# Kernel tuning notes

Measured on AMD Instinct MI355X. Metric: run time of the kernel, lower is better.

Reference implementation:

```python
import jax, jax.numpy as jnp
import numpy as np

N, E, B = 250000, 1000000, 500
FD = 78  # num_features_xd


def setup_inputs() -> dict:
    key = jax.random.key(0)
    ks = jax.random.split(key, 24)
    g = lambda i, shape, fan_in: jax.random.normal(ks[i], shape, jnp.float32) / np.sqrt(fan_in)
    inp = {
        "x": jax.random.normal(ks[0], (N, FD), jnp.float32),
        "edge_index": jax.random.randint(ks[1], (2, E), 0, N, jnp.int32),
        "batch": jnp.repeat(jnp.arange(B, dtype=jnp.int32), N // B),  # sorted, every graph non-empty
        "target": jax.random.randint(ks[2], (B, 1000), 0, 26, jnp.int32),
        # GCN layers
        "W1": g(3, (FD, FD), FD), "b1": jnp.zeros((FD,), jnp.float32),
        "W2": g(4, (FD, 2 * FD), FD), "b2": jnp.zeros((2 * FD,), jnp.float32),
        "W3": g(5, (2 * FD, 4 * FD), 2 * FD), "b3": jnp.zeros((4 * FD,), jnp.float32),
        # graph head
        "fcg1_w": g(6, (4 * FD, 1024), 4 * FD), "fcg1_b": jnp.zeros((1024,), jnp.float32),
        "fcg2_w": g(7, (1024, 128), 1024), "fcg2_b": jnp.zeros((128,), jnp.float32),
        # protein branch
        "emb": g(8, (26, 128), 1),
        "conv_w": g(9, (32, 1000, 8), 1000 * 8), "conv_b": jnp.zeros((32,), jnp.float32),
        "fcxt_w": g(10, (32 * 121, 128), 32 * 121), "fcxt_b": jnp.zeros((128,), jnp.float32),
        # fusion head
        "fc1_w": g(11, (256, 1024), 256), "fc1_b": jnp.zeros((1024,), jnp.float32),
        "fc2_w": g(12, (1024, 512), 1024), "fc2_b": jnp.zeros((512,), jnp.float32),
        "out_w": g(13, (512, 1), 512), "out_b": jnp.zeros((1,), jnp.float32),
    }
    return inp


def _gcn_conv(x, W, b, src, dst, dinv, n):
    # PyG GCNConv: out = D^-1/2 (A+I) D^-1/2 (x W) + b, symmetric norm with self-loops
    xw = x @ W
    norm = dinv[src] * dinv[dst]                                   # [E]
    agg = jax.ops.segment_sum(xw[src] * norm[:, None], dst, num_segments=n)
    agg = agg + xw * (dinv * dinv)[:, None]                        # self-loop term
    return agg + b


def reference(x, edge_index, batch, target,
              W1, b1, W2, b2, W3, b3,
              fcg1_w, fcg1_b, fcg2_w, fcg2_b,
              emb, conv_w, conv_b, fcxt_w, fcxt_b,
              fc1_w, fc1_b, fc2_w, fc2_b, out_w, out_b):
    n = x.shape[0]
    src, dst = edge_index[0], edge_index[1]
    # degree with self-loops (edge weights 1)
    deg = jax.ops.segment_sum(jnp.ones((src.shape[0],), x.dtype), dst, num_segments=n) + 1.0
    dinv = jax.lax.rsqrt(deg)

    h = jax.nn.relu(_gcn_conv(x, W1, b1, src, dst, dinv, n))
    h = jax.nn.relu(_gcn_conv(h, W2, b2, src, dst, dinv, n))
    h = jax.nn.relu(_gcn_conv(h, W3, b3, src, dst, dinv, n))

    bsz = fcg2_w.shape[1] * 0 + target.shape[0]  # B
    g = jax.ops.segment_max(h, batch, num_segments=bsz)            # global max pool -> [B, 312]
    g = jax.nn.relu(g @ fcg1_w + fcg1_b)
    g = g @ fcg2_w + fcg2_b                                        # dropout = identity (eval)

    # protein branch: Conv1d over embedding dim (channels = seq positions = 1000)
    e = emb[target]                                                # [B, 1000, 128]
    c = jax.lax.conv_general_dilated(e, conv_w, window_strides=(1,), padding="VALID",
                                     dimension_numbers=("NCH", "OIH", "NCH"))
    c = c + conv_b[None, :, None]                                  # [B, 32, 121]
    xt = c.reshape(bsz, 32 * 121) @ fcxt_w + fcxt_b

    xc = jnp.concatenate([g, xt], axis=1)                          # [B, 256]
    xc = jax.nn.relu(xc @ fc1_w + fc1_b)
    xc = jax.nn.relu(xc @ fc2_w + fc2_b)
    return xc @ out_w + out_b                                      # [B, 1]
```

## Files before the change

### kernel.cpp

```cpp
#include <hip/hip_runtime.h>
#include <hip/hip_bf16.h>

#define DEV_INLINE __device__ __forceinline__

static constexpr int Nn = 250000;
static constexpr int Ee = 1000000;
static constexpr int Bb = 500;
static constexpr int NPB = Nn / Bb;

typedef __attribute__((ext_vector_type(8))) short short8;
typedef __attribute__((ext_vector_type(8))) unsigned short ushort8v;
typedef __attribute__((ext_vector_type(4))) unsigned int uint4v;
typedef __attribute__((ext_vector_type(4))) float f32x4;
typedef __attribute__((ext_vector_type(2))) float f32x2;

DEV_INLINE __hip_bfloat16 f2b(float v) { return __float2bfloat16(v); }
DEV_INLINE unsigned short f2bu(float v) {
    __hip_bfloat16 h = __float2bfloat16(v);
    return __builtin_bit_cast(unsigned short, h);
}

DEV_INLINE f32x2 pairf(unsigned u) {
    f32x2 r;
    r.x = __uint_as_float(u << 16);
    r.y = __uint_as_float(u & 0xffff0000u);
    return r;
}
DEV_INLINE f32x2 fma2(f32x2 a, f32x2 b, f32x2 c) {
#if __has_builtin(__builtin_elementwise_fma)
    return __builtin_elementwise_fma(a, b, c);
#else
    return a * b + c;
#endif
}

__global__ void k_deg(const int* __restrict__ dst, int* __restrict__ deg) {
    int i = blockIdx.x * 256 + threadIdx.x;
    if (i < Ee) atomicAdd(&deg[dst[i]], 1);
}

__global__ void k_dinv(const int* __restrict__ deg, float* __restrict__ dinv) {
    int i = blockIdx.x * 256 + threadIdx.x;
    if (i < Nn) dinv[i] = rsqrtf((float)deg[i] + 1.0f);
}

__global__ __launch_bounds__(256) void k_scan1(const int* __restrict__ deg,
                                               int* __restrict__ rp,
                                               int* __restrict__ bsum) {
    __shared__ int s[256];
    int t = threadIdx.x;
    int i = blockIdx.x * 256 + t;
    int v = (i < Nn) ? deg[i] : 0;
    s[t] = v;
    __syncthreads();
    for (int off = 1; off < 256; off <<= 1) {
        int x = (t >= off) ? s[t - off] : 0;
        __syncthreads();
        s[t] += x;
        __syncthreads();
    }
    if (i < Nn) rp[i] = s[t] - v;
    if (t == 255) bsum[blockIdx.x] = s[255];
}

__global__ __launch_bounds__(1024) void k_scan2(int* __restrict__ bsum, int nb) {
    __shared__ int s[1024];
    int t = threadIdx.x;
    int v = (t < nb) ? bsum[t] : 0;
    s[t] = v;
    __syncthreads();
    for (int off = 1; off < 1024; off <<= 1) {
        int x = (t >= off) ? s[t - off] : 0;
        __syncthreads();
        s[t] += x;
        __syncthreads();
    }
    if (t < nb) bsum[t] = s[t] - v;
}

__global__ void k_scan3(int* __restrict__ rp, int* __restrict__ cursor,
                        const int* __restrict__ bsum) {
    int i = blockIdx.x * 256 + threadIdx.x;
    if (i < Nn) {
        int v = rp[i] + bsum[blockIdx.x];
        rp[i] = v;
        cursor[i] = v;
    }
    if (i == 0) rp[Nn] = Ee;
}

__global__ void k_scatter(const int* __restrict__ src, const int* __restrict__ dst,
                          const float* __restrict__ dinv, int* __restrict__ cursor,
                          int* __restrict__ col, float* __restrict__ enorm) {
    int i = blockIdx.x * 256 + threadIdx.x;
    if (i >= Ee) return;
    int s = src[i], d = dst[i];
    int pos = atomicAdd(&cursor[d], 1);
    col[pos] = s;
    enorm[pos] = dinv[s] * dinv[d];
}

__global__ void k_xprep(const float* __restrict__ x, unsigned short* __restrict__ xb) {
    int gid = blockIdx.x * 256 + threadIdx.x;
    if (gid >= Nn * 20) return;
    int i = gid / 20;
    int c = gid - 20 * i;
    int k = 4 * c;
    const float* xp = x + (size_t)i * 78;
    ushort4 u;
    u.x = (k + 0 < 78) ? f2bu(xp[k + 0]) : (unsigned short)0;
    u.y = (k + 1 < 78) ? f2bu(xp[k + 1]) : (unsigned short)0;
    u.z = (k + 2 < 78) ? f2bu(xp[k + 2]) : (unsigned short)0;
    u.w = (k + 3 < 78) ? f2bu(xp[k + 3]) : (unsigned short)0;
    *(ushort4*)&xb[(size_t)i * 80 + k] = u;
}

template <int K, int F, int KP, int FP>
__global__ __launch_bounds__(64) void k_wprep(const float* __restrict__ W,
                                              unsigned short* __restrict__ Wb) {
    constexpr int KSTEPS = KP / 32;
    const int nt = blockIdx.x, ks = blockIdx.y;
    const int l = threadIdx.x;
    const int n = nt * 16 + (l & 15);
    unsigned short* o = Wb + ((size_t)(nt * KSTEPS + ks) * 64 + l) * 8;
#pragma unroll
    for (int j = 0; j < 8; ++j) {
        const int k = (l >> 4) * 8 + j + ks * 32;
        o[j] = (k < K && n < F) ? f2bu(W[(size_t)k * F + n]) : (unsigned short)0;
    }
}

template <int KIN, int KP, int F, int FP, int SOUT, bool POOL, int MAXROWS>
__global__ __launch_bounds__(320, 8) void k_gcn(const __hip_bfloat16* __restrict__ in_,
                                                const int* __restrict__ rp,
                                                const int* __restrict__ col,
                                                const float* __restrict__ enorm,
                                                const float* __restrict__ dinv,
                                                const unsigned short* __restrict__ Wb,
                                                const float* __restrict__ bias,
                                                __hip_bfloat16* __restrict__ out,
                                                float* __restrict__ gpool) {
    constexpr int BD = 320, WAVES = 5;
    constexpr int CPR = KIN / 8;
    constexpr int ECAP = 16 * MAXROWS;
    constexpr int KSTEPS = KP / 32;
    constexpr int NT = FP / 16;
    constexpr int TPW = NT / WAVES;
    static_assert(KIN % 8 == 0 && KP % 32 == 0 && KP >= KIN && FP % (16 * WAVES) == 0, "pad");
    static_assert(MAXROWS % 16 == 0, "row tiles");
    static_assert(!POOL || MAXROWS == 16, "pool path assumes 16 rows");
    static_assert(CPR * MAXROWS == BD, "one slot per thread");
    const unsigned short* in = (const unsigned short*)in_;

    __shared__ alignas(16) unsigned short sh[MAXROWS * KP];
    __shared__ int sRp[MAXROWS + 1];
    __shared__ int sCol[ECAP];
    __shared__ float sEn[ECAP];

    const int i0 = blockIdx.x * MAXROWS;
    const int rows = min(MAXROWS, Nn - i0);
    const int t = threadIdx.x;
    const int slots = rows * CPR;
    const bool act = (t < slots);

    const int r = t / CPR;
    const int c = t - r * CPR;
    const size_t coff = (size_t)8 * c;
    uint4v selfv = {0u, 0u, 0u, 0u};
    float selfw = 0.f;
    if (act) {
        const int i = i0 + r;
        selfv = *(const uint4v*)(in + (size_t)i * KIN + coff);
        const float di = dinv[i];
        selfw = di * di;
    }

    if (t <= rows) sRp[t] = rp[i0 + t];
    const int base = rp[i0];
    const int ne = rp[i0 + rows] - base;
    const bool fit = (ne <= ECAP);
    if (fit) {
        for (int e = t; e < ne; e += BD) {
            sCol[e] = col[base + e];
            sEn[e] = enorm[base + e];
        }
    }
    if constexpr (KP > KIN) {
        for (int e = t; e < MAXROWS * (KP - KIN); e += BD) {
            const int rr = e / (KP - KIN);
            sh[rr * KP + KIN + (e - rr * (KP - KIN))] = 0;
        }
    }
    __syncthreads();

    if (act) {
        f32x2 acc2[4];
#pragma unroll
        for (int q = 0; q < 4; ++q) acc2[q] = pairf(selfv[q]) * selfw;

        const int e0a = sRp[r], e1a = sRp[r + 1];
        if (fit) {
            int j = e0a - base;
            const int jend = e1a - base;
            const int jm = jend - 1;
            for (; j < jend; j += 8) {
                int jj[8];
                float wv[8];
#pragma unroll
                for (int q = 0; q < 8; ++q) {
                    jj[q] = min(j + q, jm);
                    wv[q] = (j + q < jend) ? sEn[jj[q]] : 0.f;
                }
                uint4v a[8];
#pragma unroll
                for (int q = 0; q < 8; ++q)
                    a[q] = *(const uint4v*)(in + (size_t)sCol[jj[q]] * KIN + coff);
#pragma unroll
                for (int q = 0; q < 8; ++q) {
                    const f32x2 wq = {wv[q], wv[q]};
#pragma unroll
                    for (int p = 0; p < 4; ++p)
                        acc2[p] = fma2(pairf(a[q][p]), wq, acc2[p]);
                }
            }
        } else {
            for (int j = e0a; j < e1a; ++j) {
                const int n = col[j];
                const float wv = enorm[j];
                const f32x2 wvv = {wv, wv};
                uint4v a = *(const uint4v*)(in + (size_t)n * KIN + coff);
#pragma unroll
                for (int q = 0; q < 4; ++q) acc2[q] = fma2(pairf(a[q]), wvv, acc2[q]);
            }
        }
        ushort8v o;
#pragma unroll
        for (int q = 0; q < 4; ++q) {
            o[2 * q + 0] = f2bu(acc2[q].x);
            o[2 * q + 1] = f2bu(acc2[q].y);
        }
        *(ushort8v*)&sh[r * KP + 8 * c] = o;
    }
    __syncthreads();

    const int w = t >> 6, lane = t & 63;
    const int arow = lane & 15, aquad = lane >> 4;
    const int nrt = rows >> 4;

    for (int rt = 0; rt < nrt; ++rt) {
        short8 afr[KSTEPS];
#pragma unroll
        for (int ks = 0; ks < KSTEPS; ++ks)
            afr[ks] = *(const short8*)&sh[(rt * 16 + arow) * KP + aquad * 8 + ks * 32];

        const int ir0 = i0 + rt * 16;
        const bool uni = (ir0 / NPB) == ((ir0 + 15) / NPB);

#pragma unroll
        for (int nti = 0; nti < TPW; ++nti) {
            const int nt = w * TPW + nti;
            const short8* bp = (const short8*)Wb + (size_t)nt * KSTEPS * 64 + lane;
            f32x4 acc = {0.f, 0.f, 0.f, 0.f};
#pragma unroll
            for (int ks = 0; ks < KSTEPS; ++ks) {
                short8 bfr = bp[ks * 64];
                acc = __builtin_amdgcn_mfma_f32_16x16x32_bf16(afr[ks], bfr, acc, 0, 0, 0);
            }
            const int f = nt * 16 + arow;
            const int ib = ir0 + aquad * 4;
            if constexpr (!POOL) {
                if (f < F) {
                    const float bv = bias[f];
#pragma unroll
                    for (int rr = 0; rr < 4; ++rr)
                        out[(size_t)(ib + rr) * SOUT + f] = f2b(fmaxf(acc[rr] + bv, 0.f));
                } else if (f < SOUT) {
#pragma unroll
                    for (int rr = 0; rr < 4; ++rr)
                        out[(size_t)(ib + rr) * SOUT + f] = f2b(0.f);
                }
            } else {
                float m = 0.f, v[4];
                const float bv = (f < F) ? bias[f] : 0.f;
#pragma unroll
                for (int rr = 0; rr < 4; ++rr) {
                    v[rr] = fmaxf(acc[rr] + bv, 0.f);
                    m = fmaxf(m, v[rr]);
                }
                if (uni) {
                    m = fmaxf(m, __shfl_xor(m, 16));
                    m = fmaxf(m, __shfl_xor(m, 32));
                    if (aquad == 0 && f < F)
                        atomicMax((int*)&gpool[(ir0 / NPB) * F + f], __float_as_int(m));
                } else if (f < F) {
                    const int g0 = ib / NPB, g3 = (ib + 3) / NPB;
                    if (g0 == g3) {
                        atomicMax((int*)&gpool[g0 * F + f], __float_as_int(m));
                    } else {
#pragma unroll
                        for (int rr = 0; rr < 4; ++rr)
                            atomicMax((int*)&gpool[((ib + rr) / NPB) * F + f], __float_as_int(v[rr]));
                    }
                }
            }
        }
    }
}

template <int K, int FOUT, int KS, bool RELU, int BD>
__global__ __launch_bounds__(BD) void k_fc(const float* __restrict__ in,
                                           const float* __restrict__ W,
                                           const float* __restrict__ bias,
                                           float* __restrict__ out,
                                           int ostride, int ooff) {
    static_assert(!(RELU && KS > 1), "cannot split K with fused ReLU");
    static_assert(K % KS == 0, "K must divide evenly");
    constexpr int KC = K / KS;
    const int j = blockIdx.x * BD + threadIdx.x;
    const int b = blockIdx.y;
    const int z = blockIdx.z;
    const float* __restrict__ inp = in + (size_t)b * K + z * KC;
    const float* __restrict__ Wp = W + (size_t)(z * KC) * FOUT + j;
    float acc = (z == 0) ? bias[j] : 0.f;
#pragma unroll 8
    for (int k = 0; k < KC; ++k) acc += inp[k] * Wp[(size_t)k * FOUT];
    float* dst = &out[(size_t)b * ostride + ooff + j];
    if (KS > 1) {
        atomicAdd(dst, acc);
    } else {
        *dst = RELU ? fmaxf(acc, 0.f) : acc;
    }
}

__global__ __launch_bounds__(128) void k_P(const float* __restrict__ emb,
                                           const float* __restrict__ fcxt_w,
                                           float* __restrict__ P) {
    const int v = blockIdx.x, o = blockIdx.y;
    const int j = threadIdx.x;
    __shared__ float se[128];
    se[j] = emb[v * 128 + j];
    __syncthreads();
    float acc[8];
#pragma unroll
    for (int k = 0; k < 8; ++k) acc[k] = 0.f;
    const float* fw = fcxt_w + (size_t)(o * 121) * 128 + j;
#pragma unroll 4
    for (int h = 0; h < 121; ++h) {
        const float f = fw[(size_t)h * 128];
#pragma unroll
        for (int k = 0; k < 8; ++k) acc[k] += se[h + k] * f;
    }
    float* Pp = P + ((size_t)(v * 32 + o) * 8) * 128 + j;
#pragma unroll
    for (int k = 0; k < 8; ++k) Pp[(size_t)k * 128] = acc[k];
}

__global__ __launch_bounds__(128) void k_T(const float* __restrict__ convw,
                                           const float* __restrict__ P,
                                           float* __restrict__ T) {
    const int i0 = blockIdx.x * 8;
    const int v = blockIdx.y;
    const int t = threadIdx.x;
    __shared__ float wt[8 * 256];
    for (int e = t; e < 2048; e += 128) {
        const int r = e >> 8;
        const int kk = e & 255;
        wt[e] = convw[(size_t)(kk >> 3) * 8000 + (size_t)(i0 + r) * 8 + (kk & 7)];
    }
    __syncthreads();
    float acc[8];
#pragma unroll
    for (int r = 0; r < 8; ++r) acc[r] = 0.f;
    const float* Pp = P + (size_t)v * 256 * 128 + t;
#pragma unroll 2
    for (int kk = 0; kk < 256; ++kk) {
        const float pv = Pp[(size_t)kk * 128];
#pragma unroll
        for (int r = 0; r < 8; ++r) acc[r] += wt[r * 256 + kk] * pv;
    }
    float* Tp = T + ((size_t)v * 1000 + i0) * 128 + t;
#pragma unroll
    for (int r = 0; r < 8; ++r) Tp[(size_t)r * 128] = acc[r];
}

__global__ __launch_bounds__(128) void k_C0(const float* __restrict__ fcxt_w,
                                            const float* __restrict__ fcxt_b,
                                            const float* __restrict__ convb,
                                            float* __restrict__ C0) {
    const int o = blockIdx.x;
    const int j = threadIdx.x;
    float acc = 0.f;
    const float* fw = fcxt_w + (size_t)(o * 121) * 128 + j;
#pragma unroll 4
    for (int h = 0; h < 121; ++h) acc += fw[(size_t)h * 128];
    acc *= convb[o];
    if (o == 0) acc += fcxt_b[j];
    atomicAdd(&C0[j], acc);
}

template <int ZS>
__global__ __launch_bounds__(128) void k_xt(const int* __restrict__ target,
                                            const float* __restrict__ T,
                                            const float* __restrict__ C0,
                                            float* __restrict__ xc) {
    constexpr int CH = 1000 / ZS;
    const int b = blockIdx.x;
    const int z = blockIdx.y;
    const int j = threadIdx.x;
    const int* tg = target + b * 1000 + z * CH;
    float acc = (z == 0) ? C0[j] : 0.f;
    int i = 0;
    for (; i + 4 <= CH; i += 4) {
        const int v0 = tg[i + 0], v1 = tg[i + 1], v2 = tg[i + 2], v3 = tg[i + 3];
        const int ib = z * CH + i;
        acc += T[((size_t)v0 * 1000 + ib + 0) * 128 + j]
             + T[((size_t)v1 * 1000 + ib + 1) * 128 + j]
             + T[((size_t)v2 * 1000 + ib + 2) * 128 + j]
             + T[((size_t)v3 * 1000 + ib + 3) * 128 + j];
    }
    for (; i < CH; ++i) {
        acc += T[((size_t)tg[i] * 1000 + z * CH + i) * 128 + j];
    }
    atomicAdd(&xc[(size_t)b * 256 + 128 + j], acc);
}

__global__ __launch_bounds__(64) void k_out(const float* __restrict__ in,
                                            const float* __restrict__ w,
                                            const float* __restrict__ ob,
                                            float* __restrict__ out) {
    const int b = blockIdx.x;
    const int lane = threadIdx.x;
    const float* p = in + (size_t)b * 512;
    float acc = 0.f;
#pragma unroll
    for (int i = 0; i < 8; ++i) acc += p[lane + 64 * i] * w[lane + 64 * i];
    for (int off = 32; off > 0; off >>= 1) acc += __shfl_down(acc, off);
    if (lane == 0) out[b] = acc + ob[0];
}

extern "C" void kernel_launch(void* const* d_in, const int* in_sizes, int n_in,
                              void* d_out, int out_size, void* d_ws, size_t ws_size,
                              hipStream_t stream) {
    (void)in_sizes; (void)n_in; (void)out_size; (void)ws_size;
    const float* x      = (const float*)d_in[0];
    const int* ei       = (const int*)d_in[1];
    const int* target   = (const int*)d_in[3];
    const float* W1     = (const float*)d_in[4];
    const float* b1     = (const float*)d_in[5];
    const float* W2     = (const float*)d_in[6];
    const float* b2     = (const float*)d_in[7];
    const float* W3     = (const float*)d_in[8];
    const float* b3     = (const float*)d_in[9];
    const float* fcg1_w = (const float*)d_in[10];
    const float* fcg1_b = (const float*)d_in[11];
    const float* fcg2_w = (const float*)d_in[12];
    const float* fcg2_b = (const float*)d_in[13];
    const float* emb    = (const float*)d_in[14];
    const float* conv_w = (const float*)d_in[15];
    const float* conv_b = (const float*)d_in[16];
    const float* fcxt_w = (const float*)d_in[17];
    const float* fcxt_b = (const float*)d_in[18];
    const float* fc1_w  = (const float*)d_in[19];
    const float* fc1_b  = (const float*)d_in[20];
    const float* fc2_w  = (const float*)d_in[21];
    const float* fc2_b  = (const float*)d_in[22];
    const float* out_w  = (const float*)d_in[23];
    const float* out_b  = (const float*)d_in[24];

    const int* src = ei;
    const int* dst = ei + Ee;

    size_t off = 0;
    auto alloc = [&](size_t bytes) -> void* {
        off = (off + 255) & ~(size_t)255;
        void* p = (char*)d_ws + off;
        off += bytes;
        return p;
    };
    int*   deg    = (int*)alloc((size_t)Nn * 4);
    float* dinv   = (float*)alloc((size_t)Nn * 4);
    int*   rp     = (int*)alloc((size_t)(Nn + 1) * 4);
    int*   col    = (int*)alloc((size_t)Ee * 4);
    float* enorm  = (float*)alloc((size_t)Ee * 4);
    int*   bsum   = (int*)alloc(1024 * 4);
    unsigned short* Wb1 = (unsigned short*)alloc((size_t)5 * 3 * 64 * 8 * 2);
    unsigned short* Wb2 = (unsigned short*)alloc((size_t)10 * 3 * 64 * 8 * 2);
    unsigned short* Wb3 = (unsigned short*)alloc((size_t)20 * 5 * 64 * 8 * 2);
    __hip_bfloat16* h1 = (__hip_bfloat16*)alloc((size_t)Nn * 80 * 2);
    __hip_bfloat16* h2 = (__hip_bfloat16*)alloc((size_t)Nn * 160 * 2);
    int* cursor = deg;
    unsigned short* xb = (unsigned short*)h2;

    size_t hoff = 0;
    auto halloc = [&](size_t bytes) -> void* {
        hoff = (hoff + 255) & ~(size_t)255;
        void* p = (char*)h1 + hoff;
        hoff += bytes;
        return p;
    };
    float* gpool = (float*)halloc((size_t)Bb * 312 * 4);
    float* g1    = (float*)halloc((size_t)Bb * 1024 * 4);
    float* xc    = (float*)halloc((size_t)Bb * 256 * 4);
    float* f1    = (float*)halloc((size_t)Bb * 1024 * 4);
    float* f2    = (float*)halloc((size_t)Bb * 512 * 4);
    float* C0    = (float*)halloc(128 * 4);
    float* Pbuf  = (float*)halloc((size_t)26 * 32 * 8 * 128 * 4);
    float* Tbuf  = (float*)halloc((size_t)26 * 1000 * 128 * 4);

    const int nb = (Nn + 255) / 256;

    k_xprep<<<(Nn * 20 + 255) / 256, 256, 0, stream>>>(x, xb);

    hipMemsetAsync(deg, 0, (size_t)Nn * 4, stream);
    k_deg<<<(Ee + 255) / 256, 256, 0, stream>>>(dst, deg);
    k_dinv<<<nb, 256, 0, stream>>>(deg, dinv);
    k_scan1<<<nb, 256, 0, stream>>>(deg, rp, bsum);
    k_scan2<<<1, 1024, 0, stream>>>(bsum, nb);
    k_scan3<<<nb, 256, 0, stream>>>(rp, cursor, bsum);
    k_scatter<<<(Ee + 255) / 256, 256, 0, stream>>>(src, dst, dinv, cursor, col, enorm);

    k_wprep<78, 78, 96, 80><<<dim3(5, 3), 64, 0, stream>>>(W1, Wb1);
    k_wprep<78, 156, 96, 160><<<dim3(10, 3), 64, 0, stream>>>(W2, Wb2);
    k_wprep<156, 312, 160, 320><<<dim3(20, 5), 64, 0, stream>>>(W3, Wb3);

    const int g32 = (Nn + 31) / 32;
    k_gcn<80, 96, 78, 80, 80, false, 32><<<g32, 320, 0, stream>>>(
        (const __hip_bfloat16*)xb, rp, col, enorm, dinv, Wb1, b1, h1, (float*)nullptr);
    k_gcn<80, 96, 156, 160, 160, false, 32><<<g32, 320, 0, stream>>>(
        h1, rp, col, enorm, dinv, Wb2, b2, h2, (float*)nullptr);
    hipMemsetAsync(gpool, 0, (size_t)Bb * 312 * 4, stream);
    k_gcn<160, 160, 312, 320, 0, true, 16><<<Nn / 16, 320, 0, stream>>>(
        h2, rp, col, enorm, dinv, Wb3, b3, (__hip_bfloat16*)nullptr, gpool);

    hipMemsetAsync(C0, 0, 128 * 4, stream);
    hipMemsetAsync(xc, 0, (size_t)Bb * 256 * 4, stream);
    k_P<<<dim3(26, 32), 128, 0, stream>>>(emb, fcxt_w, Pbuf);
    k_T<<<dim3(125, 26), 128, 0, stream>>>(conv_w, Pbuf, Tbuf);
    k_C0<<<32, 128, 0, stream>>>(fcxt_w, fcxt_b, conv_b, C0);
    k_xt<8><<<dim3(Bb, 8), 128, 0, stream>>>(target, Tbuf, C0, xc);

    k_fc<312, 1024, 1, true, 256><<<dim3(4, Bb, 1), 256, 0, stream>>>(gpool, fcg1_w, fcg1_b, g1, 1024, 0);
    k_fc<1024, 128, 2, false, 128><<<dim3(1, Bb, 2), 128, 0, stream>>>(g1, fcg2_w, fcg2_b, xc, 256, 0);

    k_fc<256, 1024, 1, true, 256><<<dim3(4, Bb, 1), 256, 0, stream>>>(xc, fc1_w, fc1_b, f1, 1024, 0);
    k_fc<1024, 512, 1, true, 256><<<dim3(2, Bb, 1), 256, 0, stream>>>(f1, fc2_w, fc2_b, f2, 512, 0);
    k_out<<<Bb, 64, 0, stream>>>(f2, out_w, out_b, (float*)d_out);
}
```

Before: 835.0 us.

## Process two gather slots per thread and double GCN row tiles

The GCN kernel now lets each thread handle up to two (row, chunk) gather slots, so each block covers 64 rows for layers 1-2 and 32 rows for the pooled layer 3. The per-thread gather loop interleaves both slots in a single loop, with 4 neighbours per slot per iteration. This is meant to amortize the per-block CSR loading, syncs and the MFMA weight work over more rows, and to give more independent loads in flight. In exchange it uses more registers and shared memory, lowers the occupancy hint from 8 to 6, and adds padded iterations when the two slots have unequal degrees. The pool path, previously restricted to 16 rows, now runs with 32.

Measured after the change: 986.7 us. 1.18x slower.

```diff
diff --git a/kernel.cpp b/kernel.cpp
--- a/kernel.cpp
+++ b/kernel.cpp
@@ -131,7 +131,7 @@
 }
 
 template <int KIN, int KP, int F, int FP, int SOUT, bool POOL, int MAXROWS>
-__global__ __launch_bounds__(320, 8) void k_gcn(const __hip_bfloat16* __restrict__ in_,
+__global__ __launch_bounds__(320, 6) void k_gcn(const __hip_bfloat16* __restrict__ in_,
                                                 const int* __restrict__ rp,
                                                 const int* __restrict__ col,
                                                 const float* __restrict__ enorm,
@@ -142,14 +142,14 @@
                                                 float* __restrict__ gpool) {
     constexpr int BD = 320, WAVES = 5;
     constexpr int CPR = KIN / 8;
+    constexpr int NS = (MAXROWS * CPR) / BD;
     constexpr int ECAP = 16 * MAXROWS;
     constexpr int KSTEPS = KP / 32;
     constexpr int NT = FP / 16;
     constexpr int TPW = NT / WAVES;
     static_assert(KIN % 8 == 0 && KP % 32 == 0 && KP >= KIN && FP % (16 * WAVES) == 0, "pad");
     static_assert(MAXROWS % 16 == 0, "row tiles");
-    static_assert(!POOL || MAXROWS == 16, "pool path assumes 16 rows");
-    static_assert(CPR * MAXROWS == BD, "one slot per thread");
+    static_assert(MAXROWS * CPR == NS * BD && NS >= 1 && NS <= 2, "slot tiling");
     const unsigned short* in = (const unsigned short*)in_;
 
     __shared__ alignas(16) unsigned short sh[MAXROWS * KP];
@@ -161,18 +161,25 @@
     const int rows = min(MAXROWS, Nn - i0);
     const int t = threadIdx.x;
     const int slots = rows * CPR;
-    const bool act = (t < slots);
-
-    const int r = t / CPR;
-    const int c = t - r * CPR;
-    const size_t coff = (size_t)8 * c;
-    uint4v selfv = {0u, 0u, 0u, 0u};
-    float selfw = 0.f;
-    if (act) {
-        const int i = i0 + r;
-        selfv = *(const uint4v*)(in + (size_t)i * KIN + coff);
-        const float di = dinv[i];
-        selfw = di * di;
+
+    int rs[NS], cs[NS];
+    bool acts[NS];
+    uint4v selfv[NS];
+    float selfw[NS];
+#pragma unroll
+    for (int s = 0; s < NS; ++s) {
+        const int slot = t + s * BD;
+        acts[s] = (slot < slots);
+        rs[s] = slot / CPR;
+        cs[s] = slot - rs[s] * CPR;
+        selfv[s] = uint4v{0u, 0u, 0u, 0u};
+        selfw[s] = 0.f;
+        if (acts[s]) {
+            const int i = i0 + rs[s];
+            selfv[s] = *(const uint4v*)(in + (size_t)i * KIN + (size_t)8 * cs[s]);
+            const float di = dinv[i];
+            selfw[s] = di * di;
+        }
     }
 
     if (t <= rows) sRp[t] = rp[i0 + t];
@@ -193,53 +200,78 @@
     }
     __syncthreads();
 
-    if (act) {
-        f32x2 acc2[4];
-#pragma unroll
-        for (int q = 0; q < 4; ++q) acc2[q] = pairf(selfv[q]) * selfw;
-
-        const int e0a = sRp[r], e1a = sRp[r + 1];
-        if (fit) {
-            int j = e0a - base;
-            const int jend = e1a - base;
-            const int jm = jend - 1;
-            for (; j < jend; j += 8) {
-                int jj[8];
-                float wv[8];
-#pragma unroll
-                for (int q = 0; q < 8; ++q) {
-                    jj[q] = min(j + q, jm);
-                    wv[q] = (j + q < jend) ? sEn[jj[q]] : 0.f;
-                }
-                uint4v a[8];
-#pragma unroll
-                for (int q = 0; q < 8; ++q)
-                    a[q] = *(const uint4v*)(in + (size_t)sCol[jj[q]] * KIN + coff);
-#pragma unroll
-                for (int q = 0; q < 8; ++q) {
-                    const f32x2 wq = {wv[q], wv[q]};
-#pragma unroll
-                    for (int p = 0; p < 4; ++p)
-                        acc2[p] = fma2(pairf(a[q][p]), wq, acc2[p]);
+    f32x2 acc2[NS][4];
+    int j[NS], jend[NS];
+    int nit = 0;
+#pragma unroll
+    for (int s = 0; s < NS; ++s) {
+#pragma unroll
+        for (int q = 0; q < 4; ++q) acc2[s][q] = pairf(selfv[s][q]) * selfw[s];
+        j[s] = acts[s] ? (sRp[rs[s]] - base) : 0;
+        jend[s] = acts[s] ? (sRp[rs[s] + 1] - base) : 0;
+        const int rnd = (jend[s] - j[s] + 3) >> 2;
+        nit = max(nit, rnd);
+    }
+
+    if (fit) {
+        for (int it = 0; it < nit; ++it) {
+            int nn[NS][4];
+            float wv[NS][4];
+#pragma unroll
+            for (int s = 0; s < NS; ++s) {
+                const int jmc = max(jend[s] - 1, 0);
+#pragma unroll
+                for (int q = 0; q < 4; ++q) {
+                    const int idx = min(j[s] + q, jmc);
+                    nn[s][q] = sCol[idx];
+                    wv[s][q] = (j[s] + q < jend[s]) ? sEn[idx] : 0.f;
                 }
             }
-        } else {
-            for (int j = e0a; j < e1a; ++j) {
-                const int n = col[j];
-                const float wv = enorm[j];
-                const f32x2 wvv = {wv, wv};
-                uint4v a = *(const uint4v*)(in + (size_t)n * KIN + coff);
-#pragma unroll
-                for (int q = 0; q < 4; ++q) acc2[q] = fma2(pairf(a[q]), wvv, acc2[q]);
+            uint4v a[NS][4];
+#pragma unroll
+            for (int s = 0; s < NS; ++s)
+#pragma unroll
+                for (int q = 0; q < 4; ++q)
+                    a[s][q] = *(const uint4v*)(in + (size_t)nn[s][q] * KIN + (size_t)8 * cs[s]);
+#pragma unroll
+            for (int s = 0; s < NS; ++s)
+#pragma unroll
+                for (int q = 0; q < 4; ++q) {
+                    const f32x2 wq = {wv[s][q], wv[s][q]};
+#pragma unroll
+                    for (int p = 0; p < 4; ++p)
+                        acc2[s][p] = fma2(pairf(a[s][q][p]), wq, acc2[s][p]);
+                }
+#pragma unroll
+            for (int s = 0; s < NS; ++s) j[s] += 4;
+        }
+    } else {
+#pragma unroll
+        for (int s = 0; s < NS; ++s) {
+            if (acts[s]) {
+                for (int jj = sRp[rs[s]]; jj < sRp[rs[s] + 1]; ++jj) {
+                    const int n = col[jj];
+                    const float wvv = enorm[jj];
+                    const f32x2 wq = {wvv, wvv};
+                    uint4v a = *(const uint4v*)(in + (size_t)n * KIN + (size_t)8 * cs[s]);
+#pragma unroll
+                    for (int p = 0; p < 4; ++p) acc2[s][p] = fma2(pairf(a[p]), wq, acc2[s][p]);
+                }
             }
         }
-        ushort8v o;
-#pragma unroll
-        for (int q = 0; q < 4; ++q) {
-            o[2 * q + 0] = f2bu(acc2[q].x);
-            o[2 * q + 1] = f2bu(acc2[q].y);
-        }
-        *(ushort8v*)&sh[r * KP + 8 * c] = o;
+    }
+
+#pragma unroll
+    for (int s = 0; s < NS; ++s) {
+        if (acts[s]) {
+            ushort8v o;
+#pragma unroll
+            for (int q = 0; q < 4; ++q) {
+                o[2 * q + 0] = f2bu(acc2[s][q].x);
+                o[2 * q + 1] = f2bu(acc2[s][q].y);
+            }
+            *(ushort8v*)&sh[rs[s] * KP + 8 * cs[s]] = o;
+        }
     }
     __syncthreads();
 
@@ -523,13 +555,14 @@
     k_wprep<78, 156, 96, 160><<<dim3(10, 3), 64, 0, stream>>>(W2, Wb2);
     k_wprep<156, 312, 160, 320><<<dim3(20, 5), 64, 0, stream>>>(W3, Wb3);
 
+    const int g64 = (Nn + 63) / 64;
     const int g32 = (Nn + 31) / 32;
-    k_gcn<80, 96, 78, 80, 80, false, 32><<<g32, 320, 0, stream>>>(
+    k_gcn<80, 96, 78, 80, 80, false, 64><<<g64, 320, 0, stream>>>(
         (const __hip_bfloat16*)xb, rp, col, enorm, dinv, Wb1, b1, h1, (float*)nullptr);
-    k_gcn<80, 96, 156, 160, 160, false, 32><<<g32, 320, 0, stream>>>(
+    k_gcn<80, 96, 156, 160, 160, false, 64><<<g64, 320, 0, stream>>>(
         h1, rp, col, enorm, dinv, Wb2, b2, h2, (float*)nullptr);
     hipMemsetAsync(gpool, 0, (size_t)Bb * 312 * 4, stream);
-    k_gcn<160, 160, 312, 320, 0, true, 16><<<Nn / 16, 320, 0, stream>>>(
+    k_gcn<160, 160, 312, 320, 0, true, 32><<<g32, 320, 0, stream>>>(
         h2, rp, col, enorm, dinv, Wb3, b3, (__hip_bfloat16*)nullptr, gpool);
 
     hipMemsetAsync(C0, 0, 128 * 4, stream);
```
